# Kernel optimization log

Measured on AMD Instinct MI355X. Metric: run time of the kernel, lower is better.

Reference implementation:

```python
import jax, jax.numpy as jnp
import numpy as np

DIM, HID, BATCH = 64, 512, 8192


def setup_inputs() -> dict:
    key = jax.random.key(0)
    ks = jax.random.split(key, 6)
    s1 = 1.0 / np.sqrt(DIM + 1)
    s2 = 1.0 / np.sqrt(HID)
    return {
        "t": jax.random.uniform(ks[0], (1,), dtype=jnp.float32),
        "x": jax.random.normal(ks[1], (BATCH, DIM), dtype=jnp.float32),
        "W1": jax.random.normal(ks[2], (DIM + 1, HID), dtype=jnp.float32) * s1,
        "b1": jnp.zeros((HID,), jnp.float32),
        "W2": jax.random.normal(ks[3], (HID, HID), dtype=jnp.float32) * s2,
        "b2": jnp.zeros((HID,), jnp.float32),
        "W3": jax.random.normal(ks[4], (HID, DIM), dtype=jnp.float32) * s2,
        "b3": jnp.zeros((DIM,), jnp.float32),
    }


def _vf_single(ts, xs, W1, b1, W2, b2, W3, b3):
    # xs: [dim], ts: scalar. Time concatenated as extra input feature.
    h = jnp.concatenate([xs, ts[None]])          # [dim+1]
    h = jnp.tanh(h @ W1 + b1)                    # [hid]
    h = jnp.tanh(h @ W2 + b2)                    # [hid]
    return h @ W3 + b3                           # [dim]


def reference(t, x, W1, b1, W2, b2, W3, b3):
    ts = t[0]
    vf = lambda xs: _vf_single(ts, xs, W1, b1, W2, b2, W3, b3)
    v = jax.vmap(vf)(x)                                   # [B, dim]
    # Exact divergence: trace of per-sample Jacobian dv/dx.
    # (Replaces the torch per-dim autograd.grad loop with one batched jacfwd.)
    J = jax.vmap(jax.jacfwd(vf))(x)                       # [B, dim, dim]
    div = jnp.trace(J, axis1=-2, axis2=-1)                # [B]
    return (v, -div[:, None])
```

## Files before the change

kernel.cpp:

```cpp
#include <hip/hip_runtime.h>

#define DIM 64
#define HID 512
#define BATCH 8192
#define MB 32
#define NTHR 1024

typedef __attribute__((ext_vector_type(8))) short short8;
typedef __attribute__((ext_vector_type(4))) float f32x4;
typedef __attribute__((ext_vector_type(16))) float f32x16;
typedef float float4_ __attribute__((ext_vector_type(4)));
typedef unsigned long long ull;

#define Z16 {0.f,0.f,0.f,0.f,0.f,0.f,0.f,0.f,0.f,0.f,0.f,0.f,0.f,0.f,0.f,0.f}

union U8 { short8 s8; unsigned short u[8]; };
union U4 { ull v; unsigned short u[4]; };
union FB { unsigned u; float f; };

__device__ __forceinline__ unsigned short f2bf(float f) {
    union { float f; unsigned u; } v; v.f = f;
    return (unsigned short)((v.u + 0x7FFFu + ((v.u >> 16) & 1u)) >> 16);
}
__device__ __forceinline__ float bf2f(unsigned short b) {
    FB v; v.u = (unsigned)b << 16; return v.f;
}
__device__ __forceinline__ float tanh_fast(float x) {
    float e = __expf(2.f * x);
    return 1.f - __fdividef(2.f, e + 1.f);
}

__global__ __launch_bounds__(256) void prep(
        const float* __restrict__ t,  const float* __restrict__ W1,
        const float* __restrict__ b1, const float* __restrict__ W2,
        const float* __restrict__ W3,
        unsigned short* __restrict__ w2pk, unsigned short* __restrict__ ppk,
        unsigned short* __restrict__ w3pk, unsigned short* __restrict__ w1pk,
        float* __restrict__ c1) {
    __shared__ float w3sT[DIM * 33];
    __shared__ float w1s[DIM * DIM];
    int b = blockIdx.x;
    if (b >= 288) {
        int n = (b - 288) * 256 + threadIdx.x;
        c1[n] = fmaf(t[0], W1[DIM * HID + n], b1[n]);
        return;
    }
    int gid = b * 256 + threadIdx.x;
    int f = gid >> 6, l = gid & 63;
    if (f < 512) {
        int nt = f >> 5, ks = f & 31;
        int n = nt * 32 + (l & 31), k0 = ks * 16 + (l >> 5) * 8;
        unsigned short* o = w2pk + (size_t)(f * 64 + l) * 8;
#pragma unroll
        for (int e = 0; e < 8; ++e) o[e] = f2bf(W2[(size_t)(k0 + e) * HID + n]);
    } else if (f < 1024) {
        int ntb = (b * 4 - 512) >> 5;
        int jb  = (((b - 128) * 4) & 31) * 16;
        for (int idx = threadIdx.x; idx < 32 * DIM; idx += 256) {
            int dn = idx >> 6, i = idx & 63;
            w3sT[i * 33 + dn] = W3[(size_t)(ntb * 32 + dn) * DIM + i];
        }
        for (int idx = threadIdx.x; idx < DIM * DIM; idx += 256) {
            int i = idx >> 6, jj = idx & 63;
            w1s[i * DIM + jj] = W1[(size_t)i * HID + jb + jj];
        }
        __syncthreads();
        int fi = f - 512;
        int ks = fi & 31;
        int dn = l & 31, k0 = ks * 16 + (l >> 5) * 8;
        int n = ntb * 32 + dn;
        int jo = k0 - jb;
        float m[8] = {0.f,0.f,0.f,0.f,0.f,0.f,0.f,0.f};
#pragma unroll
        for (int i = 0; i < DIM; ++i) {
            float w3 = w3sT[i * 33 + dn];
            const float* wrow = &w1s[i * DIM + jo];
#pragma unroll
            for (int e = 0; e < 8; ++e) m[e] = fmaf(wrow[e], w3, m[e]);
        }
        unsigned short* o = ppk + (size_t)(fi * 64 + l) * 8;
#pragma unroll
        for (int e = 0; e < 8; ++e) o[e] = f2bf(W2[(size_t)(k0 + e) * HID + n] * m[e]);
    } else if (f < 1088) {
        int fi = f - 1024;
        int nt = fi >> 4, ks = fi & 15;
        int n = nt * 16 + (l & 15), k0 = ks * 32 + (l >> 4) * 8;
        unsigned short* o = w3pk + (size_t)(fi * 64 + l) * 8;
#pragma unroll
        for (int e = 0; e < 8; ++e) o[e] = f2bf(W3[(size_t)(k0 + e) * DIM + n]);
    } else {
        int fi = f - 1088;
        int nt = fi >> 1, ks = fi & 1;
        int n = nt * 16 + (l & 15), k0 = ks * 32 + (l >> 4) * 8;
        unsigned short* o = w1pk + (size_t)(fi * 64 + l) * 8;
#pragma unroll
        for (int e = 0; e < 8; ++e) o[e] = f2bf(W1[(size_t)(k0 + e) * HID + n]);
    }
}

__device__ __forceinline__ int act_addr(int sample, int colbyte) {
    return (sample * 1024 + colbyte) ^ ((sample & 15) << 4);
}

__global__ __launch_bounds__(NTHR) void fused_main(
        const float* __restrict__ x,  const float* __restrict__ c1,
        const float* __restrict__ b2, const float* __restrict__ b3,
        const unsigned short* __restrict__ w1pk, const unsigned short* __restrict__ w2pk,
        const unsigned short* __restrict__ ppk,  const unsigned short* __restrict__ w3pk,
        float* __restrict__ out) {
    __shared__ unsigned short h1s[MB * HID];
    __shared__ unsigned short d1s[MB * HID];
    __shared__ unsigned short h2s[MB * HID];
    __shared__ float sdump[8 * 16 * 64];
    __shared__ float wred[8][MB];
    char* h1b = (char*)h1s; char* d1b = (char*)d1s; char* h2b = (char*)h2s;

    const int tid = threadIdx.x, w = tid >> 6, l = tid & 63;
    const int lr = l & 15, g = l >> 4;
    const int s0 = blockIdx.x * MB;

    short8 xf[2][2];
#pragma unroll
    for (int nt = 0; nt < 2; ++nt)
#pragma unroll
        for (int ks = 0; ks < 2; ++ks) {
            const float* xp = x + (size_t)(s0 + nt * 16 + lr) * DIM + ks * 32 + g * 8;
            float4_ x0 = *(const float4_*)xp;
            float4_ x1 = *(const float4_*)(xp + 4);
            U8 u;
            u.u[0]=f2bf(x0.x); u.u[1]=f2bf(x0.y); u.u[2]=f2bf(x0.z); u.u[3]=f2bf(x0.w);
            u.u[4]=f2bf(x1.x); u.u[5]=f2bf(x1.y); u.u[6]=f2bf(x1.z); u.u[7]=f2bf(x1.w);
            xf[nt][ks] = u.s8;
        }
#pragma unroll
    for (int mi = 0; mi < 2; ++mi) {
        int mt = w * 2 + mi;
        short8 a0 = ((const short8*)w1pk)[(size_t)((mt * 2 + 0) * 64 + l)];
        short8 a1 = ((const short8*)w1pk)[(size_t)((mt * 2 + 1) * 64 + l)];
        float c1q[4];
#pragma unroll
        for (int r = 0; r < 4; ++r) c1q[r] = c1[mt * 16 + g * 4 + r];
#pragma unroll
        for (int nt = 0; nt < 2; ++nt) {
            f32x4 acc = {0.f, 0.f, 0.f, 0.f};
            acc = __builtin_amdgcn_mfma_f32_16x16x32_bf16(a0, xf[nt][0], acc, 0, 0, 0);
            acc = __builtin_amdgcn_mfma_f32_16x16x32_bf16(a1, xf[nt][1], acc, 0, 0, 0);
            int sample = nt * 16 + lr;
            U4 hu, du;
#pragma unroll
            for (int r = 0; r < 4; ++r) {
                float h = tanh_fast(acc[r] + c1q[r]);
                hu.u[r] = f2bf(h);
                du.u[r] = f2bf(fmaf(-h, h, 1.f));
            }
            int ab = act_addr(sample, (mt * 16 + g * 4) * 2);
            *(ull*)(h1b + ab) = hu.v;
            *(ull*)(d1b + ab) = du.v;
        }
    }
    __syncthreads();

    const int q = w & 7, role = w >> 3;
    const short8* Bbase = (const short8*)(role ? ppk : w2pk);
    const char* Ab = role ? d1b : h1b;
    f32x16 s1 = Z16;

#pragma unroll
    for (int j = 0; j < 2; ++j) {
        const int nt = 2 * q + j;
        const short8* bs = Bbase + (size_t)(nt * 32) * 64 + l;
        f32x16 acc = Z16;
#pragma unroll 2
        for (int ks = 0; ks < 32; ++ks) {
            short8 av = *(const short8*)(Ab + act_addr(l & 31, ks * 32 + (l >> 5) * 16));
            acc = __builtin_amdgcn_mfma_f32_32x32x16_bf16(av, bs[ks * 64], acc, 0, 0, 0);
        }
        if (role == 0) {
            int c = nt * 32 + (l & 31);
            float b2v = b2[c];
#pragma unroll
            for (int r = 0; r < 16; ++r) {
                int row = (r & 3) + 8 * (r >> 2) + 4 * (l >> 5);
                *(unsigned short*)(h2b + act_addr(row, c * 2)) = f2bf(tanh_fast(acc[r] + b2v));
            }
        } else if (j == 0) {
#pragma unroll
            for (int r = 0; r < 16; ++r) sdump[(q * 16 + r) * 64 + l] = acc[r];
        } else {
            s1 = acc;
        }
    }
    __syncthreads();

    if (role == 1) {
        float divp[16];
        int c0 = (2 * q) * 32 + (l & 31), c1c = c0 + 32;
#pragma unroll
        for (int r = 0; r < 16; ++r) {
            int row = (r & 3) + 8 * (r >> 2) + 4 * (l >> 5);
            float h2a = bf2f(*(const unsigned short*)(h2b + act_addr(row, c0 * 2)));
            float h2c = bf2f(*(const unsigned short*)(h2b + act_addr(row, c1c * 2)));
            float s0v = sdump[(q * 16 + r) * 64 + l];
            divp[r] = s0v * fmaf(-h2a, h2a, 1.f) + s1[r] * fmaf(-h2c, h2c, 1.f);
        }
#pragma unroll
        for (int off = 1; off < 32; off <<= 1) {
#pragma unroll
            for (int r = 0; r < 16; ++r) divp[r] += __shfl_xor(divp[r], off, 64);
        }
        if ((l & 31) == 0) {
#pragma unroll
            for (int r = 0; r < 16; ++r) {
                int row = (r & 3) + 8 * (r >> 2) + 4 * (l >> 5);
                wred[q][row] = divp[r];
            }
        }
    } else {
        const int wm3 = w & 1, wn3 = w >> 1;
        f32x4 acc = {0.f, 0.f, 0.f, 0.f};
        const short8* W3f = (const short8*)w3pk + (size_t)(wn3 * 16) * 64 + l;
#pragma unroll
        for (int ks = 0; ks < 16; ++ks) {
            short8 ah = *(const short8*)(h2b + act_addr(wm3 * 16 + lr, ks * 64 + g * 16));
            acc = __builtin_amdgcn_mfma_f32_16x16x32_bf16(ah, W3f[ks * 64], acc, 0, 0, 0);
        }
        int c = wn3 * 16 + lr;
        float b3v = b3[c];
#pragma unroll
        for (int r = 0; r < 4; ++r)
            out[(size_t)(s0 + wm3 * 16 + g * 4 + r) * DIM + c] = acc[r] + b3v;
    }
    __syncthreads();
    if (tid < MB) {
        float d = 0.f;
#pragma unroll
        for (int ww = 0; ww < 8; ++ww) d += wred[ww][tid];
        out[(size_t)BATCH * DIM + s0 + tid] = -d;
    }
}

extern "C" void kernel_launch(void* const* d_in, const int* in_sizes, int n_in,
                              void* d_out, int out_size, void* d_ws, size_t ws_size,
                              hipStream_t stream) {
    const float* t  = (const float*)d_in[0];
    const float* x  = (const float*)d_in[1];
    const float* W1 = (const float*)d_in[2];
    const float* b1 = (const float*)d_in[3];
    const float* W2 = (const float*)d_in[4];
    const float* b2 = (const float*)d_in[5];
    const float* W3 = (const float*)d_in[6];
    const float* b3 = (const float*)d_in[7];
    float* out = (float*)d_out;

    char* ws = (char*)d_ws;
    unsigned short* w2pk = (unsigned short*)ws;
    unsigned short* ppk  = (unsigned short*)(ws + (512 << 10));
    unsigned short* w3pk = (unsigned short*)(ws + (1 << 20));
    unsigned short* w1pk = (unsigned short*)(ws + (1 << 20) + (64 << 10));
    float*          c1   = (float*)(ws + (1 << 20) + (128 << 10));

    prep<<<290, 256, 0, stream>>>(t, W1, b1, W2, W3, w2pk, ppk, w3pk, w1pk, c1);
    fused_main<<<BATCH / MB, NTHR, 0, stream>>>(x, c1, b2, b3, w1pk, w2pk, ppk, w3pk, out);
}
```

Measured before the change: 33.89 us.

## Halve block to 512 threads, keep all tangent accumulators in registers

```diff
diff --git a/kernel.cpp b/kernel.cpp
--- a/kernel.cpp
+++ b/kernel.cpp
@@ -4,7 +4,7 @@
 #define HID 512
 #define BATCH 8192
 #define MB 32
-#define NTHR 1024
+#define NTHR 512
 
 typedef __attribute__((ext_vector_type(8))) short short8;
 typedef __attribute__((ext_vector_type(4))) float f32x4;
@@ -102,7 +102,9 @@
     return (sample * 1024 + colbyte) ^ ((sample & 15) << 4);
 }
 
-__global__ __launch_bounds__(NTHR) void fused_main(
+__global__ __launch_bounds__(NTHR)
+__attribute__((amdgpu_waves_per_eu(2, 2)))
+void fused_main(
         const float* __restrict__ x,  const float* __restrict__ c1,
         const float* __restrict__ b2, const float* __restrict__ b3,
         const unsigned short* __restrict__ w1pk, const unsigned short* __restrict__ w2pk,
@@ -111,8 +113,7 @@
     __shared__ unsigned short h1s[MB * HID];
     __shared__ unsigned short d1s[MB * HID];
     __shared__ unsigned short h2s[MB * HID];
-    __shared__ float sdump[8 * 16 * 64];
-    __shared__ float wred[8][MB];
+    __shared__ float wred[4][MB];
     char* h1b = (char*)h1s; char* d1b = (char*)d1s; char* h2b = (char*)h2s;
 
     const int tid = threadIdx.x, w = tid >> 6, l = tid & 63;
@@ -133,8 +134,8 @@
             xf[nt][ks] = u.s8;
         }
 #pragma unroll
-    for (int mi = 0; mi < 2; ++mi) {
-        int mt = w * 2 + mi;
+    for (int mi = 0; mi < 4; ++mi) {
+        int mt = w * 4 + mi;
         short8 a0 = ((const short8*)w1pk)[(size_t)((mt * 2 + 0) * 64 + l)];
         short8 a1 = ((const short8*)w1pk)[(size_t)((mt * 2 + 1) * 64 + l)];
         float c1q[4];
@@ -160,49 +161,55 @@
     }
     __syncthreads();
 
-    const int q = w & 7, role = w >> 3;
-    const short8* Bbase = (const short8*)(role ? ppk : w2pk);
+    const int q = w & 3, role = w >> 2;
+    const short8* Bf = (const short8*)(role ? ppk : w2pk);
     const char* Ab = role ? d1b : h1b;
-    f32x16 s1 = Z16;
-
-#pragma unroll
-    for (int j = 0; j < 2; ++j) {
-        const int nt = 2 * q + j;
-        const short8* bs = Bbase + (size_t)(nt * 32) * 64 + l;
-        f32x16 acc = Z16;
-#pragma unroll 2
-        for (int ks = 0; ks < 32; ++ks) {
-            short8 av = *(const short8*)(Ab + act_addr(l & 31, ks * 32 + (l >> 5) * 16));
-            acc = __builtin_amdgcn_mfma_f32_32x32x16_bf16(av, bs[ks * 64], acc, 0, 0, 0);
-        }
-        if (role == 0) {
-            int c = nt * 32 + (l & 31);
-            float b2v = b2[c];
-#pragma unroll
-            for (int r = 0; r < 16; ++r) {
-                int row = (r & 3) + 8 * (r >> 2) + 4 * (l >> 5);
-                *(unsigned short*)(h2b + act_addr(row, c * 2)) = f2bf(tanh_fast(acc[r] + b2v));
-            }
-        } else if (j == 0) {
-#pragma unroll
-            for (int r = 0; r < 16; ++r) sdump[(q * 16 + r) * 64 + l] = acc[r];
-        } else {
-            s1 = acc;
-        }
+    f32x16 k0_ = Z16, k1_ = Z16, k2_ = Z16, k3_ = Z16;
+#define KPASS(KK, J)                                                              \
+    {                                                                             \
+        const short8* bp = Bf + (size_t)((q * 4 + (J)) * 32) * 64 + l;            \
+        _Pragma("unroll 8")                                                       \
+        for (int ks = 0; ks < 32; ++ks) {                                         \
+            short8 av = *(const short8*)(Ab + act_addr(l & 31, ks * 32 + (l >> 5) * 16)); \
+            KK = __builtin_amdgcn_mfma_f32_32x32x16_bf16(av, bp[ks * 64], KK, 0, 0, 0);   \
+        }                                                                         \
+    }
+    KPASS(k0_, 0) KPASS(k1_, 1) KPASS(k2_, 2) KPASS(k3_, 3)
+#undef KPASS
+
+    if (role == 0) {
+#define ZEPI(KK, J)                                                               \
+        {                                                                         \
+            int c = (q * 4 + (J)) * 32 + (l & 31);                                \
+            float b2v = b2[c];                                                    \
+            _Pragma("unroll")                                                     \
+            for (int r = 0; r < 16; ++r) {                                        \
+                int row = (r & 3) + 8 * (r >> 2) + 4 * (l >> 5);                  \
+                *(unsigned short*)(h2b + act_addr(row, c * 2)) =                  \
+                    f2bf(tanh_fast(KK[r] + b2v));                                 \
+            }                                                                     \
+        }
+        ZEPI(k0_, 0) ZEPI(k1_, 1) ZEPI(k2_, 2) ZEPI(k3_, 3)
+#undef ZEPI
     }
     __syncthreads();
 
     if (role == 1) {
         float divp[16];
-        int c0 = (2 * q) * 32 + (l & 31), c1c = c0 + 32;
-#pragma unroll
-        for (int r = 0; r < 16; ++r) {
-            int row = (r & 3) + 8 * (r >> 2) + 4 * (l >> 5);
-            float h2a = bf2f(*(const unsigned short*)(h2b + act_addr(row, c0 * 2)));
-            float h2c = bf2f(*(const unsigned short*)(h2b + act_addr(row, c1c * 2)));
-            float s0v = sdump[(q * 16 + r) * 64 + l];
-            divp[r] = s0v * fmaf(-h2a, h2a, 1.f) + s1[r] * fmaf(-h2c, h2c, 1.f);
-        }
+#pragma unroll
+        for (int r = 0; r < 16; ++r) divp[r] = 0.f;
+#define SEPI(KK, J)                                                               \
+        {                                                                         \
+            int c = (q * 4 + (J)) * 32 + (l & 31);                                \
+            _Pragma("unroll")                                                     \
+            for (int r = 0; r < 16; ++r) {                                        \
+                int row = (r & 3) + 8 * (r >> 2) + 4 * (l >> 5);                  \
+                float h2 = bf2f(*(const unsigned short*)(h2b + act_addr(row, c * 2))); \
+                divp[r] = fmaf(KK[r], fmaf(-h2, h2, 1.f), divp[r]);               \
+            }                                                                     \
+        }
+        SEPI(k0_, 0) SEPI(k1_, 1) SEPI(k2_, 2) SEPI(k3_, 3)
+#undef SEPI
 #pragma unroll
         for (int off = 1; off < 32; off <<= 1) {
 #pragma unroll
@@ -216,25 +223,27 @@
             }
         }
     } else {
-        const int wm3 = w & 1, wn3 = w >> 1;
-        f32x4 acc = {0.f, 0.f, 0.f, 0.f};
-        const short8* W3f = (const short8*)w3pk + (size_t)(wn3 * 16) * 64 + l;
-#pragma unroll
-        for (int ks = 0; ks < 16; ++ks) {
-            short8 ah = *(const short8*)(h2b + act_addr(wm3 * 16 + lr, ks * 64 + g * 16));
-            acc = __builtin_amdgcn_mfma_f32_16x16x32_bf16(ah, W3f[ks * 64], acc, 0, 0, 0);
-        }
-        int c = wn3 * 16 + lr;
-        float b3v = b3[c];
-#pragma unroll
-        for (int r = 0; r < 4; ++r)
-            out[(size_t)(s0 + wm3 * 16 + g * 4 + r) * DIM + c] = acc[r] + b3v;
+#pragma unroll
+        for (int jj = 0; jj < 2; ++jj) {
+            int p = q * 2 + jj;
+            int wm3 = p >> 2, wn3 = p & 3;
+            f32x4 acc = {0.f, 0.f, 0.f, 0.f};
+            const short8* W3f = (const short8*)w3pk + (size_t)(wn3 * 16) * 64 + l;
+#pragma unroll
+            for (int ks = 0; ks < 16; ++ks) {
+                short8 ah = *(const short8*)(h2b + act_addr(wm3 * 16 + lr, ks * 64 + g * 16));
+                acc = __builtin_amdgcn_mfma_f32_16x16x32_bf16(ah, W3f[ks * 64], acc, 0, 0, 0);
+            }
+            int c = wn3 * 16 + lr;
+            float b3v = b3[c];
+#pragma unroll
+            for (int r = 0; r < 4; ++r)
+                out[(size_t)(s0 + wm3 * 16 + g * 4 + r) * DIM + c] = acc[r] + b3v;
+        }
     }
     __syncthreads();
     if (tid < MB) {
-        float d = 0.f;
-#pragma unroll
-        for (int ww = 0; ww < 8; ++ww) d += wred[ww][tid];
+        float d = wred[0][tid] + wred[1][tid] + wred[2][tid] + wred[3][tid];
         out[(size_t)BATCH * DIM + s0 + tid] = -d;
     }
 }
```

After: 40.69 us. 20.1% more time.
